# Performance work log

Measured on AMD Instinct MI355X. Metric: run time of the kernel, lower is better.

Reference implementation:

```python
import jax, jax.numpy as jnp
import numpy as np

B, N, M = 8, 512, 512
HID = 64  # weight_net hidden width


def setup_inputs() -> dict:
    key = jax.random.key(0)
    ks = jax.random.split(key, 8)
    pos1 = jax.random.normal(ks[0], (B, N, 3), dtype=jnp.float32)
    pos2 = jax.random.normal(ks[1], (B, M, 3), dtype=jnp.float32)
    match_scores = jax.random.uniform(ks[2], (B, N, M), dtype=jnp.float32)
    K = jax.random.normal(ks[3], (B, 3, 3), dtype=jnp.float32)
    # weight_net params: Linear(1,64) -> ReLU -> Linear(64,1) -> Sigmoid
    w1 = jax.random.normal(ks[4], (1, HID), dtype=jnp.float32) * 0.5
    b1 = jax.random.normal(ks[5], (HID,), dtype=jnp.float32) * 0.1
    w2 = jax.random.normal(ks[6], (HID, 1), dtype=jnp.float32) * 0.2
    b2 = jax.random.normal(ks[7], (1,), dtype=jnp.float32) * 0.1
    return {"pos1": pos1, "pos2": pos2, "match_scores": match_scores, "K": K,
            "w1": w1, "b1": b1, "w2": w2, "b2": b2}


def reference(pos1, pos2, match_scores, K, w1, b1, w2, b2):
    # threshold mask: score > 0.1 * per-batch max
    max_s = jnp.max(match_scores, axis=(1, 2))                     # [B]
    mask = match_scores > (0.1 * max_s)[:, None, None]             # [B,N,M]
    count = mask.sum(axis=(1, 2))                                  # [B]

    # weight_net applied to every score; masked pairs get weight 0
    h = jax.nn.relu(match_scores[..., None] * w1[0] + b1)          # [B,N,M,64]
    w = jax.nn.sigmoid(jnp.einsum('bnmh,h->bnm', h, w2[:, 0]) + b2[0])
    w = jnp.where(mask, w, 0.0)
    w = w / (jnp.sum(w, axis=(1, 2), keepdims=True) + 1e-8)        # [B,N,M]

    # weighted centroids
    wn = w.sum(axis=2)                                             # [B,N]
    wm = w.sum(axis=1)                                             # [B,M]
    c1 = jnp.einsum('bn,bnd->bd', wn, pos1)                        # [B,3]
    c2 = jnp.einsum('bm,bmd->bd', wm, pos2)                        # [B,3]

    p1c = pos1 - c1[:, None, :]                                    # [B,N,3]
    p2c = pos2 - c2[:, None, :]                                    # [B,M,3]

    # weighted cross-covariance H = sum_{n,m} w_nm * p1c_n p2c_m^T (two-step, small intermediate)
    A = jnp.einsum('bnm,bnd->bmd', w, p1c)                         # [B,M,3]
    H = jnp.einsum('bmd,bme->bde', A, p2c)                         # [B,3,3]

    # Kabsch: R = V diag(1,1,d) U^T, d = sign(det(V U^T))
    U, S, Vt = jnp.linalg.svd(H)
    V = jnp.swapaxes(Vt, -1, -2)
    det = jnp.linalg.det(jnp.matmul(V, jnp.swapaxes(U, -1, -2)))
    d = jnp.where(det < 0, -1.0, 1.0)
    dvec = jnp.stack([jnp.ones_like(d), jnp.ones_like(d), d], axis=-1)  # [B,3]
    R = jnp.einsum('bik,bk,bjk->bij', V, dvec, U)                  # [B,3,3]

    t = c2 - jnp.einsum('bij,bj->bi', R, c1)                       # [B,3]
    t = t / jnp.maximum(jnp.linalg.norm(t, axis=-1, keepdims=True), 1e-12)

    # fallback when fewer than 5 matches: R = I, t = [0,0,1]
    ok = count >= 5
    R = jnp.where(ok[:, None, None], R, jnp.eye(3, dtype=R.dtype))
    t = jnp.where(ok[:, None], t, jnp.array([0.0, 0.0, 1.0], dtype=t.dtype))
    return R, t
```

## Files before the change

kernel.cpp:

```cpp
#include <hip/hip_runtime.h>
#include <math.h>

#define BB 8
#define NN 512
#define MM 512
#define HID 64
#define TBL_N 2048

#define WS_BLKMAX 0
#define WS_TBL    256
#define WS_CNTP   (WS_TBL + 2*TBL_N)
#define WS_PART   (WS_CNTP + 512)

__device__ __forceinline__ float wredSum(float v){
  #pragma unroll
  for (int off=32; off; off>>=1) v += __shfl_xor(v, off);
  return v;
}
__device__ __forceinline__ float wredMax(float v){
  #pragma unroll
  for (int off=32; off; off>>=1) v = fmaxf(v, __shfl_xor(v, off));
  return v;
}
__device__ __forceinline__ int seg_lookup(const float* stb, float s){
  int k = (stb[31] < s) ? 32 : 0;
  k += (stb[k+15] < s) ? 16 : 0;
  k += (stb[k+7]  < s) ? 8  : 0;
  k += (stb[k+3]  < s) ? 4  : 0;
  k += (stb[k+1]  < s) ? 2  : 0;
  k += (stb[k]    < s) ? 1  : 0;
  if (k == 63 && stb[63] < s) k = 64;
  return k;
}

__global__ __launch_bounds__(256) void k_prep(const float* __restrict__ sc,
    const float* __restrict__ w1, const float* __restrict__ b1,
    const float* __restrict__ w2, const float* __restrict__ b2,
    float* __restrict__ ws)
{
  __shared__ float sred[4];
  __shared__ float traw[64], stb[64], sApos[64], sAneg[64], sBpos[64], sBneg[64];
  __shared__ float sAseg[65], sBseg[65];
  __shared__ float Gt[TBL_N+1];
  __shared__ float sconst;
  const int t = threadIdx.x;

  if (blockIdx.x == 0){
    float tp=0.f, aC=0.f, bC=0.f, cC=0.f; int cls=2;
    if (t < HID){
      float wv1=w1[t], bv1=b1[t], wv2=w2[t];
      aC = wv2*wv1; bC = wv2*bv1;
      if (wv1 > 0.f){ cls=0; tp=-bv1/wv1; }
      else if (wv1 < 0.f){ cls=1; tp=-bv1/wv1; }
      else { cls=2; tp=-1e30f; cC = wv2*fmaxf(bv1,0.f); }
      traw[t]=tp;
    }
    __syncthreads();
    if (t < HID){
      int r=0;
      for (int j=0;j<HID;++j){
        float tj=traw[j];
        r += (tj<tp || (tj==tp && j<t)) ? 1 : 0;
      }
      stb[r]=tp;
      sApos[r]=(cls==0)?aC:0.f; sAneg[r]=(cls==1)?aC:0.f;
      sBpos[r]=(cls==0)?bC:0.f; sBneg[r]=(cls==1)?bC:0.f;
      float cCs = wredSum(cC);
      if (t==0) sconst = cCs + b2[0];
    }
    __syncthreads();
    if (t==0){
      float totNA=0.f, totNB=0.f;
      for (int k=0;k<HID;++k){ totNA+=sAneg[k]; totNB+=sBneg[k]; }
      float Apos=0.f, Bpos=0.f, Aneg=totNA, Bneg=totNB;
      for (int k=0;k<=HID;++k){
        sAseg[k]=Apos+Aneg; sBseg[k]=Bpos+Bneg+sconst;
        if (k<HID){ Apos+=sApos[k]; Aneg-=sAneg[k]; Bpos+=sBpos[k]; Bneg-=sBneg[k]; }
      }
    }
    __syncthreads();
    {
      const float hstep = 1.f/(float)TBL_N;
      int j0 = t*8;
      int k = seg_lookup(stb, (float)j0*hstep);
      #pragma unroll
      for (int u=0;u<8;++u){
        int j=j0+u; float x=(float)j*hstep;
        while (k<HID && stb[k]<x) ++k;
        Gt[j]=fmaf(sAseg[k],x,sBseg[k]);
      }
      if (t==255){
        float x=1.f;
        while (k<HID && stb[k]<x) ++k;
        Gt[TBL_N]=fmaf(sAseg[k],x,sBseg[k]);
      }
    }
    __syncthreads();
    {
      float2* tbl=(float2*)(ws+WS_TBL);
      const float hstep=1.f/(float)TBL_N;
      #pragma unroll
      for (int u=0;u<8;++u){
        int j=t*8+u;
        float A=(Gt[j+1]-Gt[j])*(float)TBL_N;
        float Bc=Gt[j]-A*((float)j*hstep);
        tbl[j]=make_float2(A,Bc);
      }
    }
  } else {
    const int bid=blockIdx.x-1, b=bid>>5, chunk=bid&31;
    const float4* p=(const float4*)(sc+(size_t)b*NN*MM)+(size_t)chunk*2048+t;
    float m=0.f;
    #pragma unroll
    for (int i=0;i<8;++i){
      float4 v=p[i*256];
      m=fmaxf(m, fmaxf(fmaxf(v.x,v.y), fmaxf(v.z,v.w)));
    }
    m=wredMax(m);
    if ((t&63)==0) sred[t>>6]=m;
    __syncthreads();
    if (t==0) ws[WS_BLKMAX+bid]=fmaxf(fmaxf(sred[0],sred[1]),fmaxf(sred[2],sred[3]));
  }
}

__global__ __launch_bounds__(256) void k_stats(const float* __restrict__ sc,
    const float* __restrict__ pos1, float* __restrict__ ws)
{
  __shared__ float2 stab[TBL_N];
  __shared__ float sp1[768];
  __shared__ float wredm[4][8][9];
  __shared__ float sthr;
  const int t=threadIdx.x, bid=blockIdx.x;
  const int b=bid>>6, r=bid&63, mt=r>>1, half=r&1;
  const int m0=mt*16, n0=half*256;

  { const float4* src=(const float4*)(ws+WS_TBL);
    float4* dst=(float4*)stab;
    dst[t]=src[t]; dst[t+256]=src[t+256]; dst[t+512]=src[t+512]; dst[t+768]=src[t+768]; }
  { const float* src=pos1+((size_t)(b*NN+n0))*3;
    sp1[t]=src[t]; sp1[t+256]=src[t+256]; sp1[t+512]=src[t+512]; }
  if (t<64){
    float v=(t<32)? ws[WS_BLKMAX+b*32+t] : 0.f;
    v=wredMax(v);
    if (t==0) sthr=0.1f*v;
  }
  __syncthreads();

  const float thr=sthr;
  const int cp=t&7, rl=t>>3;
  const float2* srow=(const float2*)(sc+((size_t)(b*NN+n0))*MM+m0);
  float a0=0.f,x0=0.f,y0=0.f,z0=0.f, a1=0.f,x1=0.f,y1=0.f,z1=0.f;
  int cnt=0;
  #pragma unroll
  for (int k=0;k<8;++k){
    const int nl=rl+32*k;
    float2 s=srow[nl*256+cp];
    int i0=min((int)(s.x*(float)TBL_N),TBL_N-1);
    int i1=min((int)(s.y*(float)TBL_N),TBL_N-1);
    float2 ab0=stab[i0], ab1=stab[i1];
    float g0=fmaf(ab0.x,s.x,ab0.y);
    float g1=fmaf(ab1.x,s.y,ab1.y);
    float v0=1.f/(1.f+__expf(-g0));
    float v1=1.f/(1.f+__expf(-g1));
    bool msk0=s.x>thr, msk1=s.y>thr;
    float w0=msk0?v0:0.f, w1v=msk1?v1:0.f;
    cnt += (int)msk0 + (int)msk1;
    float px=sp1[nl*3], py=sp1[nl*3+1], pz=sp1[nl*3+2];
    a0+=w0;  x0=fmaf(w0,px,x0);  y0=fmaf(w0,py,y0);  z0=fmaf(w0,pz,z0);
    a1+=w1v; x1=fmaf(w1v,px,x1); y1=fmaf(w1v,py,y1); z1=fmaf(w1v,pz,z1);
  }
  float vals[9]={a0,x0,y0,z0,a1,x1,y1,z1,(float)cnt};
  #pragma unroll
  for (int j=0;j<9;++j){
    float v=vals[j];
    v+=__shfl_xor(v,8); v+=__shfl_xor(v,16); v+=__shfl_xor(v,32);
    vals[j]=v;
  }
  const int lane=t&63, wv=t>>6;
  if (lane<8){
    #pragma unroll
    for (int j=0;j<9;++j) wredm[wv][lane][j]=vals[j];
  }
  __syncthreads();
  if (t<64){
    const int c=t>>2, st=t&3, cpp=c>>1, odd=c&1;
    float sum=wredm[0][cpp][odd*4+st]+wredm[1][cpp][odd*4+st]
             +wredm[2][cpp][odd*4+st]+wredm[3][cpp][odd*4+st];
    ws[WS_PART + bid*64 + t]=sum;
  } else if (t==64){
    float csum=0.f;
    #pragma unroll
    for (int w=0;w<4;++w)
      #pragma unroll
      for (int c8=0;c8<8;++c8) csum+=wredm[w][c8][8];
    ws[WS_CNTP+bid]=csum;
  }
}

template<int K>
__device__ __forceinline__ void bredN(float* v, float* sredN, int t){
  #pragma unroll
  for (int j=0;j<K;++j) v[j]=wredSum(v[j]);
  __syncthreads();
  if ((t&63)==0){
    #pragma unroll
    for (int j=0;j<K;++j) sredN[(t>>6)*K+j]=v[j];
  }
  __syncthreads();
  #pragma unroll
  for (int j=0;j<K;++j) v[j]=sredN[j]+sredN[K+j]+sredN[2*K+j]+sredN[3*K+j];
}

__global__ __launch_bounds__(256) void k_final(const float* __restrict__ pos2,
    const float* __restrict__ ws, float* __restrict__ out)
{
  __shared__ float sredN[4*9];
  const int b=blockIdx.x, t=threadIdx.x;

  float wm[2], p1s[2][3], p2v[2][3];
  #pragma unroll
  for (int h2=0; h2<2; ++h2){
    const int m=t+h2*256, mt=m>>4, c=m&15;
    const float* pa=ws+WS_PART+((size_t)((b*32+mt)*2))*64 + c*4;
    const float* pb=pa+64;
    wm[h2]=pa[0]+pb[0];
    p1s[h2][0]=pa[1]+pb[1]; p1s[h2][1]=pa[2]+pb[2]; p1s[h2][2]=pa[3]+pb[3];
    const float* q=pos2+((size_t)(b*MM+m))*3;
    p2v[h2][0]=q[0]; p2v[h2][1]=q[1]; p2v[h2][2]=q[2];
  }
  float cf=(t<64)? ws[WS_CNTP+b*64+t] : 0.f;

  float v8[8];
  v8[0]=wm[0]+wm[1];
  v8[1]=cf;
  v8[2]=p1s[0][0]+p1s[1][0]; v8[3]=p1s[0][1]+p1s[1][1]; v8[4]=p1s[0][2]+p1s[1][2];
  v8[5]=fmaf(wm[0],p2v[0][0],wm[1]*p2v[1][0]);
  v8[6]=fmaf(wm[0],p2v[0][1],wm[1]*p2v[1][1]);
  v8[7]=fmaf(wm[0],p2v[0][2],wm[1]*p2v[1][2]);
  bredN<8>(v8, sredN, t);

  const float S=v8[0]+1e-8f, inv=1.f/S;
  const float cntTot=v8[1];
  const float c1x=v8[2]*inv, c1y=v8[3]*inv, c1z=v8[4]*inv;
  const float c2x=v8[5]*inv, c2y=v8[6]*inv, c2z=v8[7]*inv;

  float Hv[9]={0,0,0,0,0,0,0,0,0};
  #pragma unroll
  for (int h2=0; h2<2; ++h2){
    float wn=wm[h2]*inv;
    float ax=p1s[h2][0]*inv - wn*c1x;
    float ay=p1s[h2][1]*inv - wn*c1y;
    float az=p1s[h2][2]*inv - wn*c1z;
    float qx=p2v[h2][0]-c2x, qy=p2v[h2][1]-c2y, qz=p2v[h2][2]-c2z;
    Hv[0]=fmaf(ax,qx,Hv[0]); Hv[1]=fmaf(ax,qy,Hv[1]); Hv[2]=fmaf(ax,qz,Hv[2]);
    Hv[3]=fmaf(ay,qx,Hv[3]); Hv[4]=fmaf(ay,qy,Hv[4]); Hv[5]=fmaf(ay,qz,Hv[5]);
    Hv[6]=fmaf(az,qx,Hv[6]); Hv[7]=fmaf(az,qy,Hv[7]); Hv[8]=fmaf(az,qz,Hv[8]);
  }
  bredN<9>(Hv, sredN, t);

  if (t==0){
    float Sxx=Hv[0],Sxy=Hv[1],Sxz=Hv[2];
    float Syx=Hv[3],Syy=Hv[4],Syz=Hv[5];
    float Szx=Hv[6],Szy=Hv[7],Szz=Hv[8];
    float Kq[4][4];
    Kq[0][0]=Sxx+Syy+Szz; Kq[0][1]=Syz-Szy;     Kq[0][2]=Szx-Sxz;     Kq[0][3]=Sxy-Syx;
    Kq[1][0]=Kq[0][1];    Kq[1][1]=Sxx-Syy-Szz; Kq[1][2]=Sxy+Syx;     Kq[1][3]=Szx+Sxz;
    Kq[2][0]=Kq[0][2];    Kq[2][1]=Kq[1][2];    Kq[2][2]=Syy-Sxx-Szz; Kq[2][3]=Syz+Szy;
    Kq[3][0]=Kq[0][3];    Kq[3][1]=Kq[1][3];    Kq[3][2]=Kq[2][3];    Kq[3][3]=Szz-Sxx-Syy;
    float fn=0.f;
    #pragma unroll
    for (int i=0;i<4;++i)
      #pragma unroll
      for (int j=0;j<4;++j) fn += Kq[i][j]*Kq[i][j];
    float sig=sqrtf(fn)+1e-30f;
    #pragma unroll
    for (int i=0;i<4;++i) Kq[i][i]+=sig;
    fn=0.f;
    #pragma unroll
    for (int i=0;i<4;++i)
      #pragma unroll
      for (int j=0;j<4;++j) fn += Kq[i][j]*Kq[i][j];
    float nsc=rsqrtf(fn+1e-38f);
    #pragma unroll
    for (int i=0;i<4;++i)
      #pragma unroll
      for (int j=0;j<4;++j) Kq[i][j]*=nsc;
    #pragma unroll
    for (int sqi=0;sqi<4;++sqi){
      float Bq[4][4]; float f2=0.f;
      #pragma unroll
      for (int i=0;i<4;++i)
        #pragma unroll
        for (int j=0;j<4;++j){
          float v=0.f;
          #pragma unroll
          for (int k=0;k<4;++k) v=fmaf(Kq[i][k],Kq[k][j],v);
          Bq[i][j]=v; f2+=v*v;
        }
      float isc=rsqrtf(f2+1e-38f);
      #pragma unroll
      for (int i=0;i<4;++i)
        #pragma unroll
        for (int j=0;j<4;++j) Kq[i][j]=Bq[i][j]*isc;
    }
    float q0=1.f,q1=0.31f,q2=0.67f,q3=0.93f;
    #pragma unroll
    for (int it=0;it<16;++it){
      float n0=Kq[0][0]*q0+Kq[0][1]*q1+Kq[0][2]*q2+Kq[0][3]*q3;
      float n1=Kq[1][0]*q0+Kq[1][1]*q1+Kq[1][2]*q2+Kq[1][3]*q3;
      float n2=Kq[2][0]*q0+Kq[2][1]*q1+Kq[2][2]*q2+Kq[2][3]*q3;
      float n3=Kq[3][0]*q0+Kq[3][1]*q1+Kq[3][2]*q2+Kq[3][3]*q3;
      float nn=rsqrtf(n0*n0+n1*n1+n2*n2+n3*n3+1e-38f);
      q0=n0*nn; q1=n1*nn; q2=n2*nn; q3=n3*nn;
    }
    float R00=q0*q0+q1*q1-q2*q2-q3*q3, R01=2.f*(q1*q2-q0*q3),       R02=2.f*(q1*q3+q0*q2);
    float R10=2.f*(q1*q2+q0*q3),       R11=q0*q0-q1*q1+q2*q2-q3*q3, R12=2.f*(q2*q3-q0*q1);
    float R20=2.f*(q1*q3-q0*q2),       R21=2.f*(q2*q3+q0*q1),       R22=q0*q0-q1*q1-q2*q2+q3*q3;
    float tx=c2x-(R00*c1x+R01*c1y+R02*c1z);
    float ty=c2y-(R10*c1x+R11*c1y+R12*c1z);
    float tz=c2z-(R20*c1x+R21*c1y+R22*c1z);
    float tn=sqrtf(tx*tx+ty*ty+tz*tz);
    float itn=1.f/fmaxf(tn,1e-12f);
    tx*=itn; ty*=itn; tz*=itn;
    if (cntTot < 4.5f){
      R00=1.f;R01=0.f;R02=0.f; R10=0.f;R11=1.f;R12=0.f; R20=0.f;R21=0.f;R22=1.f;
      tx=0.f; ty=0.f; tz=1.f;
    }
    float* Ro=out+b*9;
    Ro[0]=R00;Ro[1]=R01;Ro[2]=R02;Ro[3]=R10;Ro[4]=R11;Ro[5]=R12;Ro[6]=R20;Ro[7]=R21;Ro[8]=R22;
    float* to=out+BB*9+b*3;
    to[0]=tx; to[1]=ty; to[2]=tz;
  }
}

extern "C" void kernel_launch(void* const* d_in, const int* in_sizes, int n_in,
                              void* d_out, int out_size, void* d_ws, size_t ws_size,
                              hipStream_t stream){
  const float* pos1=(const float*)d_in[0];
  const float* pos2=(const float*)d_in[1];
  const float* sc  =(const float*)d_in[2];
  const float* w1  =(const float*)d_in[4];
  const float* b1  =(const float*)d_in[5];
  const float* w2  =(const float*)d_in[6];
  const float* b2  =(const float*)d_in[7];
  float* ws=(float*)d_ws;
  float* out=(float*)d_out;

  k_prep <<<dim3(257), dim3(256), 0, stream>>>(sc, w1, b1, w2, b2, ws);
  k_stats<<<dim3(512), dim3(256), 0, stream>>>(sc, pos1, ws);
  k_final<<<dim3(BB),  dim3(256), 0, stream>>>(pos2, ws, out);
}
```

Baseline: 93.19 us.

## Fuse final Kabsch stage into stats kernel via last-block atomic counter

Removes the separate k_final launch: each k_stats block bumps a per-batch atomic counter, and the last block for a batch runs the centroid, covariance and SVD finalisation. This saves one kernel launch and its gap. It also halves the piecewise-linear sigmoid table, which shrinks its shared-memory footprint and staging copy at some cost in approximation accuracy, and uses a hardware reciprocal for the sigmoid. The atomic counters are reset in k_prep, and the fused path relies on threadfences for visibility of the partial sums.

Measured after the change: 124.5 us. 1.34x slower.

```diff
diff --git a/kernel.cpp b/kernel.cpp
--- a/kernel.cpp
+++ b/kernel.cpp
@@ -5,12 +5,13 @@
 #define NN 512
 #define MM 512
 #define HID 64
-#define TBL_N 2048
+#define TBL_N 1024
 
 #define WS_BLKMAX 0
 #define WS_TBL    256
 #define WS_CNTP   (WS_TBL + 2*TBL_N)
-#define WS_PART   (WS_CNTP + 512)
+#define WS_DONE   (WS_CNTP + 512)
+#define WS_PART   (WS_DONE + 8)
 
 __device__ __forceinline__ float wredSum(float v){
   #pragma unroll
@@ -46,6 +47,7 @@
   const int t = threadIdx.x;
 
   if (blockIdx.x == 0){
+    if (t < 8) ((unsigned*)(ws + WS_DONE))[t] = 0u;
     float tp=0.f, aC=0.f, bC=0.f, cC=0.f; int cls=2;
     if (t < HID){
       float wv1=w1[t], bv1=b1[t], wv2=w2[t];
@@ -81,10 +83,10 @@
     __syncthreads();
     {
       const float hstep = 1.f/(float)TBL_N;
-      int j0 = t*8;
+      int j0 = t*4;
       int k = seg_lookup(stb, (float)j0*hstep);
       #pragma unroll
-      for (int u=0;u<8;++u){
+      for (int u=0;u<4;++u){
         int j=j0+u; float x=(float)j*hstep;
         while (k<HID && stb[k]<x) ++k;
         Gt[j]=fmaf(sAseg[k],x,sBseg[k]);
@@ -100,8 +102,8 @@
       float2* tbl=(float2*)(ws+WS_TBL);
       const float hstep=1.f/(float)TBL_N;
       #pragma unroll
-      for (int u=0;u<8;++u){
-        int j=t*8+u;
+      for (int u=0;u<4;++u){
+        int j=t*4+u;
         float A=(Gt[j+1]-Gt[j])*(float)TBL_N;
         float Bc=Gt[j]-A*((float)j*hstep);
         tbl[j]=make_float2(A,Bc);
@@ -123,20 +125,37 @@
   }
 }
 
+template<int K>
+__device__ __forceinline__ void bredN(float* v, float* sredN, int t){
+  #pragma unroll
+  for (int j=0;j<K;++j) v[j]=wredSum(v[j]);
+  __syncthreads();
+  if ((t&63)==0){
+    #pragma unroll
+    for (int j=0;j<K;++j) sredN[(t>>6)*K+j]=v[j];
+  }
+  __syncthreads();
+  #pragma unroll
+  for (int j=0;j<K;++j) v[j]=sredN[j]+sredN[K+j]+sredN[2*K+j]+sredN[3*K+j];
+}
+
 __global__ __launch_bounds__(256) void k_stats(const float* __restrict__ sc,
-    const float* __restrict__ pos1, float* __restrict__ ws)
+    const float* __restrict__ pos1, const float* __restrict__ pos2,
+    float* __restrict__ ws, float* __restrict__ out)
 {
   __shared__ float2 stab[TBL_N];
   __shared__ float sp1[768];
   __shared__ float wredm[4][8][9];
   __shared__ float sthr;
+  __shared__ int slast;
+  __shared__ float sredN[4*9];
   const int t=threadIdx.x, bid=blockIdx.x;
   const int b=bid>>6, r=bid&63, mt=r>>1, half=r&1;
   const int m0=mt*16, n0=half*256;
 
   { const float4* src=(const float4*)(ws+WS_TBL);
     float4* dst=(float4*)stab;
-    dst[t]=src[t]; dst[t+256]=src[t+256]; dst[t+512]=src[t+512]; dst[t+768]=src[t+768]; }
+    dst[t]=src[t]; dst[t+256]=src[t+256]; }
   { const float* src=pos1+((size_t)(b*NN+n0))*3;
     sp1[t]=src[t]; sp1[t+256]=src[t+256]; sp1[t+512]=src[t+512]; }
   if (t<64){
@@ -160,8 +179,8 @@
     float2 ab0=stab[i0], ab1=stab[i1];
     float g0=fmaf(ab0.x,s.x,ab0.y);
     float g1=fmaf(ab1.x,s.y,ab1.y);
-    float v0=1.f/(1.f+__expf(-g0));
-    float v1=1.f/(1.f+__expf(-g1));
+    float v0=__builtin_amdgcn_rcpf(1.f+__expf(-g0));
+    float v1=__builtin_amdgcn_rcpf(1.f+__expf(-g1));
     bool msk0=s.x>thr, msk1=s.y>thr;
     float w0=msk0?v0:0.f, w1v=msk1?v1:0.f;
     cnt += (int)msk0 + (int)msk1;
@@ -195,33 +214,22 @@
       for (int c8=0;c8<8;++c8) csum+=wredm[w][c8][8];
     ws[WS_CNTP+bid]=csum;
   }
-}
-
-template<int K>
-__device__ __forceinline__ void bredN(float* v, float* sredN, int t){
-  #pragma unroll
-  for (int j=0;j<K;++j) v[j]=wredSum(v[j]);
-  __syncthreads();
-  if ((t&63)==0){
-    #pragma unroll
-    for (int j=0;j<K;++j) sredN[(t>>6)*K+j]=v[j];
-  }
-  __syncthreads();
-  #pragma unroll
-  for (int j=0;j<K;++j) v[j]=sredN[j]+sredN[K+j]+sredN[2*K+j]+sredN[3*K+j];
-}
-
-__global__ __launch_bounds__(256) void k_final(const float* __restrict__ pos2,
-    const float* __restrict__ ws, float* __restrict__ out)
-{
-  __shared__ float sredN[4*9];
-  const int b=blockIdx.x, t=threadIdx.x;
+
+  __threadfence();
+  __syncthreads();
+  if (t==0){
+    unsigned old = atomicAdd(((unsigned*)(ws+WS_DONE)) + b, 1u);
+    slast = (old == 63u) ? 1 : 0;
+  }
+  __syncthreads();
+  if (!slast) return;
+  __threadfence();
 
   float wm[2], p1s[2][3], p2v[2][3];
   #pragma unroll
   for (int h2=0; h2<2; ++h2){
-    const int m=t+h2*256, mt=m>>4, c=m&15;
-    const float* pa=ws+WS_PART+((size_t)((b*32+mt)*2))*64 + c*4;
+    const int m=t+h2*256, mtt=m>>4, c=m&15;
+    const float* pa=ws+WS_PART+((size_t)(b*64+mtt*2))*64 + c*4;
     const float* pb=pa+64;
     wm[h2]=pa[0]+pb[0];
     p1s[h2][0]=pa[1]+pb[1]; p1s[h2][1]=pa[2]+pb[2]; p1s[h2][2]=pa[3]+pb[3];
@@ -347,6 +355,5 @@
   float* out=(float*)d_out;
 
   k_prep <<<dim3(257), dim3(256), 0, stream>>>(sc, w1, b1, w2, b2, ws);
-  k_stats<<<dim3(512), dim3(256), 0, stream>>>(sc, pos1, ws);
-  k_final<<<dim3(BB),  dim3(256), 0, stream>>>(pos2, ws, out);
-}
+  k_stats<<<dim3(512), dim3(256), 0, stream>>>(sc, pos1, pos2, ws, out);
+}
```
